# Performance work log

Measured on AMD Instinct MI355X. Metric: run time of the kernel, lower is better.

## Reference

```python
import jax, jax.numpy as jnp
import numpy as np

B, C, T, HEADS = 4, 1024, 1024, 16


def setup_inputs() -> dict:
    key = jax.random.key(0)
    k0, k1, k2, k3 = jax.random.split(key, 4)
    x = jax.random.normal(k0, (B, C, T), dtype=jnp.float32)
    mask = jax.random.randint(k1, (B, T), 0, 2).astype(bool)  # True = masked position
    scale = 1.0 / np.sqrt(C).astype(np.float32)
    w_kvq = jax.random.normal(k2, (3 * C, C), dtype=jnp.float32) * scale  # Conv1d k=1, no bias
    w_out = jax.random.normal(k3, (C, C), dtype=jnp.float32) * scale
    return {"x": x, "mask": mask, "w_kvq": w_kvq, "w_out": w_out}


def reference(x, mask, w_kvq, w_out):
    b, c, t = x.shape
    h = HEADS
    d = c // h  # head dim; torch scales by sqrt(k.size(1)) = sqrt(d)
    # Conv1d with kernel 1 == per-timestep matmul over channels
    kvq = jnp.einsum('oc,bct->bot', w_kvq, x)  # [B, 3C, T]
    k, v, q = jnp.split(kvq, 3, axis=1)        # each [B, C, T]
    k = k.reshape(b, h, d, t)
    v = v.reshape(b, h, d, t)
    q = q.reshape(b, h, d, t)
    # att[b,h,i,j] = <k_i, q_j> / sqrt(d); i = key pos, j = query pos
    att = jnp.einsum('bhdi,bhdj->bhij', k, q) / jnp.sqrt(jnp.asarray(d, x.dtype))
    # pre-softmax: mask key positions (dim i) with -inf
    att = jnp.where(mask[:, None, :, None], -jnp.inf, att)
    att = jax.nn.softmax(att, axis=2)  # softmax over keys (torch dim=1 of [Bh,Tk,Tq])
    # post-softmax: zero out masked query positions (dim j)
    att = jnp.where(mask[:, None, None, :], jnp.asarray(0.0, x.dtype), att)
    o = jnp.einsum('bhdi,bhij->bhdj', v, att)  # [B, h, d, T]
    o = o.reshape(b, c, t)
    out = x + jnp.einsum('oc,bct->bot', w_out, o)
    # match torch layout: cat over heads along batch dim -> [h*B, T, T]
    att_flat = jnp.transpose(att, (1, 0, 2, 3)).reshape(h * b, t, t)
    return out, att_flat
```

## Files before the change

### kernel.cpp

```cpp
#include <hip/hip_runtime.h>

#define BB 4
#define CC 1024
#define TT 1024
#define HH 16
#define DD 64

typedef __bf16 v8bf __attribute__((ext_vector_type(8)));
typedef __bf16 v4bf __attribute__((ext_vector_type(4)));
typedef float  v4f  __attribute__((ext_vector_type(4)));

__device__ __forceinline__ void gl_lds16(const __bf16* g, __bf16* l) {
  __builtin_amdgcn_global_load_lds(
      (const __attribute__((address_space(1))) void*)g,
      (__attribute__((address_space(3))) void*)l, 16, 0, 0);
}

__global__ __launch_bounds__(256) void prep(
    const void* mraw, float* __restrict__ maskf,
    const float* __restrict__ w_kvq, const float* __restrict__ w_out,
    __bf16* __restrict__ wkb, __bf16* __restrict__ wob)
{
  if (blockIdx.x == 0) {
    __shared__ int flagA, flagB;
    if (threadIdx.x == 0) { flagA = 0; flagB = 0; }
    __syncthreads();
    const unsigned char* mb = (const unsigned char*)mraw;
    const int n = BB * TT;
    int a = 0, bfl = 0;
    for (int i = threadIdx.x; i < n; i += 256) {
      if (mb[i]) { if ((i & 3) == 0) a = 1; else bfl = 1; }
    }
    if (a)   atomicOr(&flagA, 1);
    if (bfl) atomicOr(&flagB, 1);
    __syncthreads();
    int layout;
    if (flagA && !flagB)      layout = 0;
    else if (!flagA && flagB) layout = 1;
    else                      layout = 2;
    for (int i = threadIdx.x; i < n; i += 256) {
      float m;
      if (layout == 0)      m = (((const int*)mraw)[i]   != 0)   ? 1.f : 0.f;
      else if (layout == 1) m = (((const float*)mraw)[i] != 0.f) ? 1.f : 0.f;
      else                  m = (mb[i] != 0)                     ? 1.f : 0.f;
      maskf[i] = m;
    }
    return;
  }
  long i = ((long)blockIdx.x - 1) * 2048 + threadIdx.x * 8;
  const float* src;
  __bf16* dst;
  if (i < (long)3 * CC * CC) { src = w_kvq + i; dst = wkb + i; }
  else { long j = i - (long)3 * CC * CC; src = w_out + j; dst = wob + j; }
  float4 f0 = *(const float4*)src;
  float4 f1 = *(const float4*)(src + 4);
  v8bf o;
  o[0] = (__bf16)f0.x; o[1] = (__bf16)f0.y; o[2] = (__bf16)f0.z; o[3] = (__bf16)f0.w;
  o[4] = (__bf16)f1.x; o[5] = (__bf16)f1.y; o[6] = (__bf16)f1.z; o[7] = (__bf16)f1.w;
  *(v8bf*)dst = o;
}

__global__ __launch_bounds__(256) void transpose_x(const float* __restrict__ x,
                                                   __bf16* __restrict__ xT) {
  const int b = blockIdx.z;
  const int t0 = blockIdx.x * 64, c0 = blockIdx.y * 64;
  __shared__ __bf16 T[64][72];
  const int tid = threadIdx.x;
  {
    int row = tid >> 2, coff = (tid & 3) * 16;
    const float* src = x + ((long)b * CC + c0 + row) * TT + t0 + coff;
#pragma unroll
    for (int s = 0; s < 4; s++) {
      float4 f = *(const float4*)(src + s * 4);
      T[row][coff + s * 4 + 0] = (__bf16)f.x;
      T[row][coff + s * 4 + 1] = (__bf16)f.y;
      T[row][coff + s * 4 + 2] = (__bf16)f.z;
      T[row][coff + s * 4 + 3] = (__bf16)f.w;
    }
  }
  __syncthreads();
  {
    int trow = tid >> 2, ccoff = (tid & 3) * 16;
    __bf16 vals[16];
#pragma unroll
    for (int i = 0; i < 16; i++) vals[i] = T[ccoff + i][trow];
    __bf16* dst = xT + ((long)b * TT + t0 + trow) * CC + c0 + ccoff;
    *(v8bf*)dst       = *(v8bf*)&vals[0];
    *(v8bf*)(dst + 8) = *(v8bf*)&vals[8];
  }
}

template <int MODE>
__global__ __launch_bounds__(256) void gemm_bt(
    const __bf16* __restrict__ A, const __bf16* __restrict__ BTfull,
    const float* __restrict__ Sfull, float* __restrict__ Ofull,
    __bf16* __restrict__ kqT, __bf16* __restrict__ vbuf,
    long strideBT)
{
  const int bz = blockIdx.z;
  const __bf16* BT = BTfull + (long)bz * strideBT;
  const int m0 = blockIdx.y * 128, n0 = blockIdx.x * 128;
  __shared__ __align__(16) char smem[(MODE == 0) ? 34816 : 16384];
  __bf16 (*As)[32] = (__bf16(*)[32])smem;
  __bf16 (*Bs)[32] = (__bf16(*)[32])(smem + 8192);
  const int tid = threadIdx.x;
  const int lane = tid & 63, wave = tid >> 6;
  const int wm = wave >> 1, wn = wave & 1;
  const int ln = lane & 15, q = lane >> 4;

  v4f acc[4][4];
#pragma unroll
  for (int i = 0; i < 4; i++)
#pragma unroll
    for (int j = 0; j < 4; j++) acc[i][j] = (v4f)(0.f);

  const int lr = lane >> 2;
  const int lc = (lane & 3) * 8;
  for (int k0 = 0; k0 < CC; k0 += 32) {
#pragma unroll
    for (int s = 0; s < 2; s++) {
      int row = wave * 32 + s * 16;
      gl_lds16(A  + (long)(m0 + row + lr) * CC + k0 + lc, &As[row][0]);
      gl_lds16(BT + (long)(n0 + row + lr) * CC + k0 + lc, &Bs[row][0]);
    }
    __syncthreads();
    v8bf af[4], bf[4];
#pragma unroll
    for (int mi = 0; mi < 4; mi++) af[mi] = *(v8bf*)&As[wm * 64 + mi * 16 + ln][q * 8];
#pragma unroll
    for (int ni = 0; ni < 4; ni++) bf[ni] = *(v8bf*)&Bs[wn * 64 + ni * 16 + ln][q * 8];
#pragma unroll
    for (int mi = 0; mi < 4; mi++)
#pragma unroll
      for (int ni = 0; ni < 4; ni++)
        acc[mi][ni] = __builtin_amdgcn_mfma_f32_16x16x32_bf16(af[mi], bf[ni], acc[mi][ni], 0, 0, 0);
    __syncthreads();
  }

  if (MODE == 1) {
#pragma unroll
    for (int mi = 0; mi < 4; mi++)
#pragma unroll
      for (int ni = 0; ni < 4; ni++)
#pragma unroll
        for (int r = 0; r < 4; r++) {
          long off = (long)bz * CC * TT + (long)(m0 + wm * 64 + mi * 16 + q * 4 + r) * TT
                   + n0 + wn * 64 + ni * 16 + ln;
          Ofull[off] = acc[mi][ni][r] + Sfull[off];
        }
  } else {
    const int third = m0 >> 10;
    if (third == 1) {
      const int mb = m0 - 1024;
#pragma unroll
      for (int mi = 0; mi < 4; mi++)
#pragma unroll
        for (int ni = 0; ni < 4; ni++)
#pragma unroll
          for (int r = 0; r < 4; r++)
            vbuf[((long)bz * CC + mb + wm * 64 + mi * 16 + q * 4 + r) * TT
                 + n0 + wn * 64 + ni * 16 + ln] = (__bf16)acc[mi][ni][r];
    } else {
      __bf16 (*Tl)[136] = (__bf16(*)[136])smem;
#pragma unroll
      for (int mi = 0; mi < 4; mi++)
#pragma unroll
        for (int ni = 0; ni < 4; ni++) {
          v4bf pb;
#pragma unroll
          for (int r = 0; r < 4; r++) pb[r] = (__bf16)acc[mi][ni][r];
          *(v4bf*)&Tl[wn * 64 + ni * 16 + ln][wm * 64 + mi * 16 + q * 4] = pb;
        }
      __syncthreads();
      const int dstbase = (third == 0) ? 0 : CC;
      const int mcol = (third == 0) ? m0 : (m0 - 2048);
      int t = tid >> 1, c0 = (tid & 1) * 64;
      __bf16* drow = kqT + ((long)bz * TT + n0 + t) * (2 * CC) + dstbase + mcol + c0;
#pragma unroll
      for (int s = 0; s < 8; s++)
        *(v8bf*)(drow + s * 8) = *(v8bf*)&Tl[t][c0 + s * 8];
    }
  }
}

__global__ __launch_bounds__(256) void attn_fstats(
    const __bf16* __restrict__ kqT, const float* __restrict__ maskf,
    float2* __restrict__ fstats)
{
  const int z = blockIdx.y, h = z >> 2, b = z & 3;
  const int j0 = blockIdx.x * 64;
  const __bf16* kbase = kqT + (long)b * TT * (2 * CC);
  const int tid = threadIdx.x;
  const int lane = tid & 63, wave = tid >> 6;
  const int ln = lane & 15, q = lane >> 4;
  __shared__ float2 red[4][64];

  v8bf bq[4][2];
#pragma unroll
  for (int ni = 0; ni < 4; ni++)
#pragma unroll
    for (int kd = 0; kd < 2; kd++)
      bq[ni][kd] = *(const v8bf*)(kbase + (long)(j0 + ni * 16 + ln) * (2 * CC)
                                  + CC + h * DD + kd * 32 + q * 8);

  float rm[4], rs[4];
#pragma unroll
  for (int ni = 0; ni < 4; ni++) { rm[ni] = -3.4e38f; rs[ni] = 0.f; }

  for (int it = 0; it < 4; it++) {
    const int ibase = wave * 256 + it * 64;
    float4 km4[4];
    v8bf ak[4][2];
#pragma unroll
    for (int mi = 0; mi < 4; mi++) {
      km4[mi] = *(const float4*)(maskf + b * TT + ibase + mi * 16 + q * 4);
#pragma unroll
      for (int kd = 0; kd < 2; kd++)
        ak[mi][kd] = *(const v8bf*)(kbase + (long)(ibase + mi * 16 + ln) * (2 * CC)
                                    + h * DD + kd * 32 + q * 8);
    }
#pragma unroll
    for (int ni = 0; ni < 4; ni++) {
      float lv[16];
      float cm = -3.4e38f;
#pragma unroll
      for (int mi = 0; mi < 4; mi++) {
        v4f l4 = (v4f)(0.f);
        l4 = __builtin_amdgcn_mfma_f32_16x16x32_bf16(ak[mi][0], bq[ni][0], l4, 0, 0, 0);
        l4 = __builtin_amdgcn_mfma_f32_16x16x32_bf16(ak[mi][1], bq[ni][1], l4, 0, 0, 0);
#pragma unroll
        for (int r = 0; r < 4; r++) {
          float km = (r == 0) ? km4[mi].x : (r == 1) ? km4[mi].y : (r == 2) ? km4[mi].z : km4[mi].w;
          float l = (km != 0.f) ? -1e30f : l4[r] * 0.125f;
          lv[mi * 4 + r] = l;
          cm = fmaxf(cm, l);
        }
      }
      float nm = fmaxf(rm[ni], cm);
      float s = 0.f;
#pragma unroll
      for (int i = 0; i < 16; i++) s += __expf(lv[i] - nm);
      rs[ni] = rs[ni] * __expf(rm[ni] - nm) + s;
      rm[ni] = nm;
    }
  }

#pragma unroll
  for (int ni = 0; ni < 4; ni++) {
    float m = rm[ni], s = rs[ni];
#pragma unroll
    for (int off = 16; off <= 32; off <<= 1) {
      float om = __shfl_xor(m, off, 64);
      float os = __shfl_xor(s, off, 64);
      float M = fmaxf(m, om);
      s = s * __expf(m - M) + os * __expf(om - M);
      m = M;
    }
    if (q == 0) red[wave][ni * 16 + ln] = make_float2(m, s);
  }
  __syncthreads();
  if (tid < 64) {
    float M = -3.4e38f;
    float2 v[4];
#pragma unroll
    for (int w = 0; w < 4; w++) { v[w] = red[w][tid]; M = fmaxf(M, v[w].x); }
    float S = 0.f;
#pragma unroll
    for (int w = 0; w < 4; w++) S += v[w].y * __expf(v[w].x - M);
    const float qz = (maskf[b * TT + j0 + tid] != 0.f) ? 0.f : 1.f;
    fstats[(long)z * TT + j0 + tid] = make_float2(M, qz / S);
  }
}

__global__ __launch_bounds__(256) void gemm_pv(
    const __bf16* __restrict__ kqT, const __bf16* __restrict__ vbuf,
    const float2* __restrict__ fstats, const float* __restrict__ maskf,
    float* __restrict__ att, __bf16* __restrict__ oT)
{
  const int z = blockIdx.y, h = z >> 2, b = z & 3;
  const int j0 = blockIdx.x * 64;
  __shared__ __align__(16) char smem[50176];
  __bf16 (*Qs)[72] = (__bf16(*)[72])smem;
  float* km = (float*)(smem + 9216 + 4 * 9216);
  const int tid = threadIdx.x;
  const int lane = tid & 63, wave = tid >> 6;
  const int ln = lane & 15, q = lane >> 4;
  __bf16 (*Pt)[72] = (__bf16(*)[72])(smem + 9216 + wave * 9216);

  const __bf16* kbase = kqT + (long)b * TT * (2 * CC);
  const __bf16* vbase = vbuf + ((long)b * CC + h * DD) * TT;

#pragma unroll
  for (int s = 0; s < 2; s++) {
    int c = tid + s * 256;
    int row = c >> 3, off = (c & 7) * 8;
    *(v8bf*)&Qs[row][off] = *(const v8bf*)(kbase + (long)(j0 + row) * (2 * CC) + CC + h * DD + off);
  }
  {
    float4 f = *(const float4*)(maskf + b * TT + tid * 4);
    *(float4*)&km[tid * 4] = f;
  }
  __syncthreads();

  v8bf bq[4][2];
#pragma unroll
  for (int ni = 0; ni < 4; ni++)
#pragma unroll
    for (int kd = 0; kd < 2; kd++)
      bq[ni][kd] = *(v8bf*)&Qs[ni * 16 + ln][kd * 32 + q * 8];
  float2 st[4];
#pragma unroll
  for (int ni = 0; ni < 4; ni++) st[ni] = fstats[(long)z * TT + j0 + ni * 16 + ln];

  v4f acc[4][4];
#pragma unroll
  for (int i = 0; i < 4; i++)
#pragma unroll
    for (int j = 0; j < 4; j++) acc[i][j] = (v4f)(0.f);

  for (int it = 0; it < 4; it++) {
    const int ibase = wave * 256 + it * 64;
#pragma unroll
    for (int mi = 0; mi < 4; mi++) {
      const __bf16* arow = kbase + (long)(ibase + mi * 16 + ln) * (2 * CC) + h * DD;
      v8bf ak0 = *(const v8bf*)(arow + q * 8);
      v8bf ak1 = *(const v8bf*)(arow + 32 + q * 8);
#pragma unroll
      for (int ni = 0; ni < 4; ni++) {
        v4f l4 = (v4f)(0.f);
        l4 = __builtin_amdgcn_mfma_f32_16x16x32_bf16(ak0, bq[ni][0], l4, 0, 0, 0);
        l4 = __builtin_amdgcn_mfma_f32_16x16x32_bf16(ak1, bq[ni][1], l4, 0, 0, 0);
        v4bf pb;
#pragma unroll
        for (int r = 0; r < 4; r++) {
          int i_loc = mi * 16 + q * 4 + r;
          int i_glob = ibase + i_loc;
          float l = (km[i_glob] != 0.f) ? -1e30f : l4[r] * 0.125f;
          float p = __expf(l - st[ni].x) * st[ni].y;
          att[((long)z << 20) + (long)i_glob * TT + j0 + ni * 16 + ln] = p;
          pb[r] = (__bf16)p;
        }
        *(v4bf*)&Pt[ni * 16 + ln][mi * 16 + q * 4] = pb;
      }
    }
    v8bf ap[4][2], bv[4][2];
#pragma unroll
    for (int ji = 0; ji < 4; ji++)
#pragma unroll
      for (int ki = 0; ki < 2; ki++)
        ap[ji][ki] = *(v8bf*)&Pt[ji * 16 + ln][ki * 32 + q * 8];
#pragma unroll
    for (int di = 0; di < 4; di++)
#pragma unroll
      for (int ki = 0; ki < 2; ki++)
        bv[di][ki] = *(const v8bf*)(vbase + (long)(di * 16 + ln) * TT + ibase + ki * 32 + q * 8);
#pragma unroll
    for (int ji = 0; ji < 4; ji++)
#pragma unroll
      for (int di = 0; di < 4; di++) {
        acc[ji][di] = __builtin_amdgcn_mfma_f32_16x16x32_bf16(ap[ji][0], bv[di][0], acc[ji][di], 0, 0, 0);
        acc[ji][di] = __builtin_amdgcn_mfma_f32_16x16x32_bf16(ap[ji][1], bv[di][1], acc[ji][di], 0, 0, 0);
      }
  }

  float (*red)[68] = (float(*)[68])(smem + 9216);
  for (int w = 0; w < 4; w++) {
    __syncthreads();
    if (wave == w) {
#pragma unroll
      for (int ji = 0; ji < 4; ji++)
#pragma unroll
        for (int di = 0; di < 4; di++)
#pragma unroll
          for (int r = 0; r < 4; r++) {
            int row = ji * 16 + q * 4 + r;
            int col = di * 16 + ln;
            if (w == 0) red[row][col] = acc[ji][di][r];
            else        red[row][col] += acc[ji][di][r];
          }
    }
  }
  __syncthreads();
  {
    int row = tid >> 2, c0 = (tid & 3) * 16;
    __bf16 ob[16];
#pragma unroll
    for (int i = 0; i < 16; i++) ob[i] = (__bf16)red[row][c0 + i];
    __bf16* dst = oT + ((long)b * TT + j0 + row) * CC + h * DD + c0;
    *(v8bf*)dst       = *(v8bf*)&ob[0];
    *(v8bf*)(dst + 8) = *(v8bf*)&ob[8];
  }
}

extern "C" void kernel_launch(void* const* d_in, const int* in_sizes, int n_in,
                              void* d_out, int out_size, void* d_ws, size_t ws_size,
                              hipStream_t stream) {
  const float* x     = (const float*)d_in[0];
  const void*  mask  = d_in[1];
  const float* w_kvq = (const float*)d_in[2];
  const float* w_out = (const float*)d_in[3];

  float* out = (float*)d_out;
  float* att = out + (long)BB * CC * TT;

  char* wsb = (char*)d_ws;
  float*   maskf = (float*)(wsb + 0);
  __bf16*  wkb   = (__bf16*)(wsb + 16384);
  __bf16*  wob   = (__bf16*)(wsb + 6307840);
  __bf16*  xT    = (__bf16*)(wsb + 8404992);
  __bf16*  kqT   = (__bf16*)(wsb + 16793600);
  __bf16*  vbuf  = (__bf16*)(wsb + 33570816);
  __bf16*  oT    = (__bf16*)(wsb + 41959424);
  float2*  fst   = (float2*)(wsb + 50348032);

  prep<<<2049, 256, 0, stream>>>(mask, maskf, w_kvq, w_out, wkb, wob);
  transpose_x<<<dim3(16, 16, BB), 256, 0, stream>>>(x, xT);
  gemm_bt<0><<<dim3(8, 24, BB), 256, 0, stream>>>(
      wkb, xT, nullptr, nullptr, kqT, vbuf, (long)CC * TT);
  attn_fstats<<<dim3(16, HH * BB), 256, 0, stream>>>(kqT, maskf, fst);
  gemm_pv<<<dim3(16, HH * BB), 256, 0, stream>>>(kqT, vbuf, fst, maskf, att, oT);
  gemm_bt<1><<<dim3(8, 8, BB), 256, 0, stream>>>(
      wob, oT, x, out, nullptr, nullptr, (long)CC * TT);
}
```

Before: 471.2 us.

## Fuse prep kernels, merge softmax stats into PV kernel, deepen GEMM K-step

Folds the x transpose into the weight-prep kernel so there is one fewer launch. It also merges the softmax-statistics pass and the PV pass into one attention kernel. In that kernel each wave owns 16 query columns and loops over all keys twice, which removes the cross-wave LDS reduction and the fstats round trip. The GEMM now stages 64-wide K slices per barrier, and the large att and out writes use nontemporal stores. The cost is that each wave recomputes QK^T twice over the full key range, and each block now has less parallel work.

```diff
diff --git a/kernel.cpp b/kernel.cpp
--- a/kernel.cpp
+++ b/kernel.cpp
@@ -16,19 +16,22 @@
       (__attribute__((address_space(3))) void*)l, 16, 0, 0);
 }
 
-__global__ __launch_bounds__(256) void prep(
+__global__ __launch_bounds__(256) void prep_all(
     const void* mraw, float* __restrict__ maskf,
     const float* __restrict__ w_kvq, const float* __restrict__ w_out,
-    __bf16* __restrict__ wkb, __bf16* __restrict__ wob)
+    __bf16* __restrict__ wkb, __bf16* __restrict__ wob,
+    const float* __restrict__ x, __bf16* __restrict__ xT)
 {
-  if (blockIdx.x == 0) {
+  const int blk = blockIdx.x;
+  const int tid = threadIdx.x;
+  if (blk == 0) {
     __shared__ int flagA, flagB;
-    if (threadIdx.x == 0) { flagA = 0; flagB = 0; }
+    if (tid == 0) { flagA = 0; flagB = 0; }
     __syncthreads();
     const unsigned char* mb = (const unsigned char*)mraw;
     const int n = BB * TT;
     int a = 0, bfl = 0;
-    for (int i = threadIdx.x; i < n; i += 256) {
+    for (int i = tid; i < n; i += 256) {
       if (mb[i]) { if ((i & 3) == 0) a = 1; else bfl = 1; }
     }
     if (a)   atomicOr(&flagA, 1);
@@ -38,7 +41,7 @@
     if (flagA && !flagB)      layout = 0;
     else if (!flagA && flagB) layout = 1;
     else                      layout = 2;
-    for (int i = threadIdx.x; i < n; i += 256) {
+    for (int i = tid; i < n; i += 256) {
       float m;
       if (layout == 0)      m = (((const int*)mraw)[i]   != 0)   ? 1.f : 0.f;
       else if (layout == 1) m = (((const float*)mraw)[i] != 0.f) ? 1.f : 0.f;
@@ -47,25 +50,24 @@
     }
     return;
   }
-  long i = ((long)blockIdx.x - 1) * 2048 + threadIdx.x * 8;
-  const float* src;
-  __bf16* dst;
-  if (i < (long)3 * CC * CC) { src = w_kvq + i; dst = wkb + i; }
-  else { long j = i - (long)3 * CC * CC; src = w_out + j; dst = wob + j; }
-  float4 f0 = *(const float4*)src;
-  float4 f1 = *(const float4*)(src + 4);
-  v8bf o;
-  o[0] = (__bf16)f0.x; o[1] = (__bf16)f0.y; o[2] = (__bf16)f0.z; o[3] = (__bf16)f0.w;
-  o[4] = (__bf16)f1.x; o[5] = (__bf16)f1.y; o[6] = (__bf16)f1.z; o[7] = (__bf16)f1.w;
-  *(v8bf*)dst = o;
-}
-
-__global__ __launch_bounds__(256) void transpose_x(const float* __restrict__ x,
-                                                   __bf16* __restrict__ xT) {
-  const int b = blockIdx.z;
-  const int t0 = blockIdx.x * 64, c0 = blockIdx.y * 64;
+  if (blk <= 2048) {
+    long i = ((long)blk - 1) * 2048 + tid * 8;
+    const float* src;
+    __bf16* dst;
+    if (i < (long)3 * CC * CC) { src = w_kvq + i; dst = wkb + i; }
+    else { long j = i - (long)3 * CC * CC; src = w_out + j; dst = wob + j; }
+    float4 f0 = *(const float4*)src;
+    float4 f1 = *(const float4*)(src + 4);
+    v8bf o;
+    o[0] = (__bf16)f0.x; o[1] = (__bf16)f0.y; o[2] = (__bf16)f0.z; o[3] = (__bf16)f0.w;
+    o[4] = (__bf16)f1.x; o[5] = (__bf16)f1.y; o[6] = (__bf16)f1.z; o[7] = (__bf16)f1.w;
+    *(v8bf*)dst = o;
+    return;
+  }
+  const int tb = blk - 2049;
+  const int b = tb >> 8;
+  const int t0 = (tb & 15) * 64, c0 = ((tb >> 4) & 15) * 64;
   __shared__ __bf16 T[64][72];
-  const int tid = threadIdx.x;
   {
     int row = tid >> 2, coff = (tid & 3) * 16;
     const float* src = x + ((long)b * CC + c0 + row) * TT + t0 + coff;
@@ -100,9 +102,9 @@
   const int bz = blockIdx.z;
   const __bf16* BT = BTfull + (long)bz * strideBT;
   const int m0 = blockIdx.y * 128, n0 = blockIdx.x * 128;
-  __shared__ __align__(16) char smem[(MODE == 0) ? 34816 : 16384];
-  __bf16 (*As)[32] = (__bf16(*)[32])smem;
-  __bf16 (*Bs)[32] = (__bf16(*)[32])(smem + 8192);
+  __shared__ __align__(16) char smem[(MODE == 0) ? 34816 : 32768];
+  __bf16 (*As)[128][32] = (__bf16(*)[128][32])smem;
+  __bf16 (*Bs)[128][32] = (__bf16(*)[128][32])(smem + 16384);
   const int tid = threadIdx.x;
   const int lane = tid & 63, wave = tid >> 6;
   const int wm = wave >> 1, wn = wave & 1;
@@ -116,24 +118,35 @@
 
   const int lr = lane >> 2;
   const int lc = (lane & 3) * 8;
-  for (int k0 = 0; k0 < CC; k0 += 32) {
+  for (int k0 = 0; k0 < CC; k0 += 64) {
 #pragma unroll
     for (int s = 0; s < 2; s++) {
       int row = wave * 32 + s * 16;
-      gl_lds16(A  + (long)(m0 + row + lr) * CC + k0 + lc, &As[row][0]);
-      gl_lds16(BT + (long)(n0 + row + lr) * CC + k0 + lc, &Bs[row][0]);
+#pragma unroll
+      for (int kd = 0; kd < 2; kd++) {
+        gl_lds16(A  + (long)(m0 + row + lr) * CC + k0 + kd * 32 + lc, &As[kd][row][0]);
+        gl_lds16(BT + (long)(n0 + row + lr) * CC + k0 + kd * 32 + lc, &Bs[kd][row][0]);
+      }
     }
     __syncthreads();
-    v8bf af[4], bf[4];
-#pragma unroll
-    for (int mi = 0; mi < 4; mi++) af[mi] = *(v8bf*)&As[wm * 64 + mi * 16 + ln][q * 8];
-#pragma unroll
-    for (int ni = 0; ni < 4; ni++) bf[ni] = *(v8bf*)&Bs[wn * 64 + ni * 16 + ln][q * 8];
+    v8bf af[4][2], bf[4][2];
 #pragma unroll
     for (int mi = 0; mi < 4; mi++)
 #pragma unroll
-      for (int ni = 0; ni < 4; ni++)
-        acc[mi][ni] = __builtin_amdgcn_mfma_f32_16x16x32_bf16(af[mi], bf[ni], acc[mi][ni], 0, 0, 0);
+      for (int kd = 0; kd < 2; kd++)
+        af[mi][kd] = *(v8bf*)&As[kd][wm * 64 + mi * 16 + ln][q * 8];
+#pragma unroll
+    for (int ni = 0; ni < 4; ni++)
+#pragma unroll
+      for (int kd = 0; kd < 2; kd++)
+        bf[ni][kd] = *(v8bf*)&Bs[kd][wn * 64 + ni * 16 + ln][q * 8];
+#pragma unroll
+    for (int mi = 0; mi < 4; mi++)
+#pragma unroll
+      for (int ni = 0; ni < 4; ni++) {
+        acc[mi][ni] = __builtin_amdgcn_mfma_f32_16x16x32_bf16(af[mi][0], bf[ni][0], acc[mi][ni], 0, 0, 0);
+        acc[mi][ni] = __builtin_amdgcn_mfma_f32_16x16x32_bf16(af[mi][1], bf[ni][1], acc[mi][ni], 0, 0, 0);
+      }
     __syncthreads();
   }
 
@@ -146,7 +159,7 @@
         for (int r = 0; r < 4; r++) {
           long off = (long)bz * CC * TT + (long)(m0 + wm * 64 + mi * 16 + q * 4 + r) * TT
                    + n0 + wn * 64 + ni * 16 + ln;
-          Ofull[off] = acc[mi][ni][r] + Sfull[off];
+          __builtin_nontemporal_store(acc[mi][ni][r] + Sfull[off], &Ofull[off]);
         }
   } else {
     const int third = m0 >> 10;
@@ -183,212 +196,114 @@
   }
 }
 
-__global__ __launch_bounds__(256) void attn_fstats(
-    const __bf16* __restrict__ kqT, const float* __restrict__ maskf,
-    float2* __restrict__ fstats)
+__global__ __launch_bounds__(256) void attn_fused(
+    const __bf16* __restrict__ kqT, const __bf16* __restrict__ vbuf,
+    const float* __restrict__ maskf, float* __restrict__ att,
+    __bf16* __restrict__ oT)
 {
   const int z = blockIdx.y, h = z >> 2, b = z & 3;
   const int j0 = blockIdx.x * 64;
-  const __bf16* kbase = kqT + (long)b * TT * (2 * CC);
   const int tid = threadIdx.x;
   const int lane = tid & 63, wave = tid >> 6;
   const int ln = lane & 15, q = lane >> 4;
-  __shared__ float2 red[4][64];
-
-  v8bf bq[4][2];
-#pragma unroll
-  for (int ni = 0; ni < 4; ni++)
-#pragma unroll
-    for (int kd = 0; kd < 2; kd++)
-      bq[ni][kd] = *(const v8bf*)(kbase + (long)(j0 + ni * 16 + ln) * (2 * CC)
-                                  + CC + h * DD + kd * 32 + q * 8);
-
-  float rm[4], rs[4];
-#pragma unroll
-  for (int ni = 0; ni < 4; ni++) { rm[ni] = -3.4e38f; rs[ni] = 0.f; }
-
-  for (int it = 0; it < 4; it++) {
-    const int ibase = wave * 256 + it * 64;
-    float4 km4[4];
-    v8bf ak[4][2];
-#pragma unroll
-    for (int mi = 0; mi < 4; mi++) {
-      km4[mi] = *(const float4*)(maskf + b * TT + ibase + mi * 16 + q * 4);
-#pragma unroll
-      for (int kd = 0; kd < 2; kd++)
-        ak[mi][kd] = *(const v8bf*)(kbase + (long)(ibase + mi * 16 + ln) * (2 * CC)
-                                    + h * DD + kd * 32 + q * 8);
-    }
-#pragma unroll
-    for (int ni = 0; ni < 4; ni++) {
-      float lv[16];
-      float cm = -3.4e38f;
-#pragma unroll
-      for (int mi = 0; mi < 4; mi++) {
-        v4f l4 = (v4f)(0.f);
-        l4 = __builtin_amdgcn_mfma_f32_16x16x32_bf16(ak[mi][0], bq[ni][0], l4, 0, 0, 0);
-        l4 = __builtin_amdgcn_mfma_f32_16x16x32_bf16(ak[mi][1], bq[ni][1], l4, 0, 0, 0);
-#pragma unroll
-        for (int r = 0; r < 4; r++) {
-          float km = (r == 0) ? km4[mi].x : (r == 1) ? km4[mi].y : (r == 2) ? km4[mi].z : km4[mi].w;
-          float l = (km != 0.f) ? -1e30f : l4[r] * 0.125f;
-          lv[mi * 4 + r] = l;
-          cm = fmaxf(cm, l);
-        }
-      }
-      float nm = fmaxf(rm[ni], cm);
-      float s = 0.f;
-#pragma unroll
-      for (int i = 0; i < 16; i++) s += __expf(lv[i] - nm);
-      rs[ni] = rs[ni] * __expf(rm[ni] - nm) + s;
-      rm[ni] = nm;
-    }
-  }
-
-#pragma unroll
-  for (int ni = 0; ni < 4; ni++) {
-    float m = rm[ni], s = rs[ni];
-#pragma unroll
-    for (int off = 16; off <= 32; off <<= 1) {
-      float om = __shfl_xor(m, off, 64);
-      float os = __shfl_xor(s, off, 64);
-      float M = fmaxf(m, om);
-      s = s * __expf(m - M) + os * __expf(om - M);
-      m = M;
-    }
-    if (q == 0) red[wave][ni * 16 + ln] = make_float2(m, s);
-  }
-  __syncthreads();
-  if (tid < 64) {
-    float M = -3.4e38f;
-    float2 v[4];
-#pragma unroll
-    for (int w = 0; w < 4; w++) { v[w] = red[w][tid]; M = fmaxf(M, v[w].x); }
-    float S = 0.f;
-#pragma unroll
-    for (int w = 0; w < 4; w++) S += v[w].y * __expf(v[w].x - M);
-    const float qz = (maskf[b * TT + j0 + tid] != 0.f) ? 0.f : 1.f;
-    fstats[(long)z * TT + j0 + tid] = make_float2(M, qz / S);
-  }
-}
-
-__global__ __launch_bounds__(256) void gemm_pv(
-    const __bf16* __restrict__ kqT, const __bf16* __restrict__ vbuf,
-    const float2* __restrict__ fstats, const float* __restrict__ maskf,
-    float* __restrict__ att, __bf16* __restrict__ oT)
-{
-  const int z = blockIdx.y, h = z >> 2, b = z & 3;
-  const int j0 = blockIdx.x * 64;
-  __shared__ __align__(16) char smem[50176];
-  __bf16 (*Qs)[72] = (__bf16(*)[72])smem;
-  float* km = (float*)(smem + 9216 + 4 * 9216);
-  const int tid = threadIdx.x;
-  const int lane = tid & 63, wave = tid >> 6;
-  const int ln = lane & 15, q = lane >> 4;
-  __bf16 (*Pt)[72] = (__bf16(*)[72])(smem + 9216 + wave * 9216);
+  __shared__ float km[1024];
+  __shared__ __bf16 PtAll[4][16][72];
 
   const __bf16* kbase = kqT + (long)b * TT * (2 * CC);
   const __bf16* vbase = vbuf + ((long)b * CC + h * DD) * TT;
-
-#pragma unroll
-  for (int s = 0; s < 2; s++) {
-    int c = tid + s * 256;
-    int row = c >> 3, off = (c & 7) * 8;
-    *(v8bf*)&Qs[row][off] = *(const v8bf*)(kbase + (long)(j0 + row) * (2 * CC) + CC + h * DD + off);
-  }
-  {
-    float4 f = *(const float4*)(maskf + b * TT + tid * 4);
-    *(float4*)&km[tid * 4] = f;
-  }
+  const int jw = j0 + wave * 16;
+
+  *(float4*)&km[tid * 4] = *(const float4*)(maskf + b * TT + tid * 4);
   __syncthreads();
 
-  v8bf bq[4][2];
-#pragma unroll
-  for (int ni = 0; ni < 4; ni++)
-#pragma unroll
-    for (int kd = 0; kd < 2; kd++)
-      bq[ni][kd] = *(v8bf*)&Qs[ni * 16 + ln][kd * 32 + q * 8];
-  float2 st[4];
-#pragma unroll
-  for (int ni = 0; ni < 4; ni++) st[ni] = fstats[(long)z * TT + j0 + ni * 16 + ln];
-
-  v4f acc[4][4];
-#pragma unroll
-  for (int i = 0; i < 4; i++)
-#pragma unroll
-    for (int j = 0; j < 4; j++) acc[i][j] = (v4f)(0.f);
-
-  for (int it = 0; it < 4; it++) {
-    const int ibase = wave * 256 + it * 64;
+  v8bf bq[2];
+#pragma unroll
+  for (int kd = 0; kd < 2; kd++)
+    bq[kd] = *(const v8bf*)(kbase + (long)(jw + ln) * (2 * CC) + CC + h * DD + kd * 32 + q * 8);
+
+  float rm = -3.4e38f, rs = 0.f;
+  for (int it = 0; it < 16; it++) {
+    const int ibase = it * 64;
+    float lv[16];
+    float cm = -3.4e38f;
 #pragma unroll
     for (int mi = 0; mi < 4; mi++) {
       const __bf16* arow = kbase + (long)(ibase + mi * 16 + ln) * (2 * CC) + h * DD;
       v8bf ak0 = *(const v8bf*)(arow + q * 8);
       v8bf ak1 = *(const v8bf*)(arow + 32 + q * 8);
-#pragma unroll
-      for (int ni = 0; ni < 4; ni++) {
-        v4f l4 = (v4f)(0.f);
-        l4 = __builtin_amdgcn_mfma_f32_16x16x32_bf16(ak0, bq[ni][0], l4, 0, 0, 0);
-        l4 = __builtin_amdgcn_mfma_f32_16x16x32_bf16(ak1, bq[ni][1], l4, 0, 0, 0);
-        v4bf pb;
-#pragma unroll
-        for (int r = 0; r < 4; r++) {
-          int i_loc = mi * 16 + q * 4 + r;
-          int i_glob = ibase + i_loc;
-          float l = (km[i_glob] != 0.f) ? -1e30f : l4[r] * 0.125f;
-          float p = __expf(l - st[ni].x) * st[ni].y;
-          att[((long)z << 20) + (long)i_glob * TT + j0 + ni * 16 + ln] = p;
-          pb[r] = (__bf16)p;
-        }
-        *(v4bf*)&Pt[ni * 16 + ln][mi * 16 + q * 4] = pb;
+      v4f l4 = (v4f)(0.f);
+      l4 = __builtin_amdgcn_mfma_f32_16x16x32_bf16(ak0, bq[0], l4, 0, 0, 0);
+      l4 = __builtin_amdgcn_mfma_f32_16x16x32_bf16(ak1, bq[1], l4, 0, 0, 0);
+#pragma unroll
+      for (int r = 0; r < 4; r++) {
+        int i = ibase + mi * 16 + q * 4 + r;
+        float l = (km[i] != 0.f) ? -1e30f : l4[r] * 0.125f;
+        lv[mi * 4 + r] = l;
+        cm = fmaxf(cm, l);
       }
     }
-    v8bf ap[4][2], bv[4][2];
-#pragma unroll
-    for (int ji = 0; ji < 4; ji++)
-#pragma unroll
-      for (int ki = 0; ki < 2; ki++)
-        ap[ji][ki] = *(v8bf*)&Pt[ji * 16 + ln][ki * 32 + q * 8];
+    float nm = fmaxf(rm, cm);
+    float s = 0.f;
+#pragma unroll
+    for (int i = 0; i < 16; i++) s += __expf(lv[i] - nm);
+    rs = rs * __expf(rm - nm) + s;
+    rm = nm;
+  }
+#pragma unroll
+  for (int off = 16; off <= 32; off <<= 1) {
+    float om = __shfl_xor(rm, off, 64);
+    float os = __shfl_xor(rs, off, 64);
+    float M = fmaxf(rm, om);
+    rs = rs * __expf(rm - M) + os * __expf(om - M);
+    rm = M;
+  }
+  const float qz = (km[jw + ln] != 0.f) ? 0.f : 1.f;
+  const float Mf = rm, iS = qz / rs;
+
+  v4f acc[4];
+#pragma unroll
+  for (int di = 0; di < 4; di++) acc[di] = (v4f)(0.f);
+  __bf16 (*Pt)[72] = PtAll[wave];
+
+  for (int it = 0; it < 16; it++) {
+    const int ibase = it * 64;
+#pragma unroll
+    for (int mi = 0; mi < 4; mi++) {
+      const __bf16* arow = kbase + (long)(ibase + mi * 16 + ln) * (2 * CC) + h * DD;
+      v8bf ak0 = *(const v8bf*)(arow + q * 8);
+      v8bf ak1 = *(const v8bf*)(arow + 32 + q * 8);
+      v4f l4 = (v4f)(0.f);
+      l4 = __builtin_amdgcn_mfma_f32_16x16x32_bf16(ak0, bq[0], l4, 0, 0, 0);
+      l4 = __builtin_amdgcn_mfma_f32_16x16x32_bf16(ak1, bq[1], l4, 0, 0, 0);
+      v4bf pb;
+#pragma unroll
+      for (int r = 0; r < 4; r++) {
+        int i = ibase + mi * 16 + q * 4 + r;
+        float l = (km[i] != 0.f) ? -1e30f : l4[r] * 0.125f;
+        float p = __expf(l - Mf) * iS;
+        __builtin_nontemporal_store(p, att + ((long)z << 20) + (long)i * TT + jw + ln);
+        pb[r] = (__bf16)p;
+      }
+      *(v4bf*)&Pt[ln][mi * 16 + q * 4] = pb;
+    }
+    v8bf ap[2];
+#pragma unroll
+    for (int kd = 0; kd < 2; kd++) ap[kd] = *(v8bf*)&Pt[ln][kd * 32 + q * 8];
+#pragma unroll
+    for (int di = 0; di < 4; di++) {
+      v8bf bv0 = *(const v8bf*)(vbase + (long)(di * 16 + ln) * TT + ibase + q * 8);
+      v8bf bv1 = *(const v8bf*)(vbase + (long)(di * 16 + ln) * TT + ibase + 32 + q * 8);
+      acc[di] = __builtin_amdgcn_mfma_f32_16x16x32_bf16(ap[0], bv0, acc[di], 0, 0, 0);
+      acc[di] = __builtin_amdgcn_mfma_f32_16x16x32_bf16(ap[1], bv1, acc[di], 0, 0, 0);
+    }
+  }
+
+#pragma unroll
+  for (int r = 0; r < 4; r++) {
+    __bf16* drow = oT + ((long)b * TT + jw + q * 4 + r) * CC + h * DD;
 #pragma unroll
     for (int di = 0; di < 4; di++)
-#pragma unroll
-      for (int ki = 0; ki < 2; ki++)
-        bv[di][ki] = *(const v8bf*)(vbase + (long)(di * 16 + ln) * TT + ibase + ki * 32 + q * 8);
-#pragma unroll
-    for (int ji = 0; ji < 4; ji++)
-#pragma unroll
-      for (int di = 0; di < 4; di++) {
-        acc[ji][di] = __builtin_amdgcn_mfma_f32_16x16x32_bf16(ap[ji][0], bv[di][0], acc[ji][di], 0, 0, 0);
-        acc[ji][di] = __builtin_amdgcn_mfma_f32_16x16x32_bf16(ap[ji][1], bv[di][1], acc[ji][di], 0, 0, 0);
-      }
-  }
-
-  float (*red)[68] = (float(*)[68])(smem + 9216);
-  for (int w = 0; w < 4; w++) {
-    __syncthreads();
-    if (wave == w) {
-#pragma unroll
-      for (int ji = 0; ji < 4; ji++)
-#pragma unroll
-        for (int di = 0; di < 4; di++)
-#pragma unroll
-          for (int r = 0; r < 4; r++) {
-            int row = ji * 16 + q * 4 + r;
-            int col = di * 16 + ln;
-            if (w == 0) red[row][col] = acc[ji][di][r];
-            else        red[row][col] += acc[ji][di][r];
-          }
-    }
-  }
-  __syncthreads();
-  {
-    int row = tid >> 2, c0 = (tid & 3) * 16;
-    __bf16 ob[16];
-#pragma unroll
-    for (int i = 0; i < 16; i++) ob[i] = (__bf16)red[row][c0 + i];
-    __bf16* dst = oT + ((long)b * TT + j0 + row) * CC + h * DD + c0;
-    *(v8bf*)dst       = *(v8bf*)&ob[0];
-    *(v8bf*)(dst + 8) = *(v8bf*)&ob[8];
+      drow[di * 16 + ln] = (__bf16)acc[di][r];
   }
 }
 
@@ -411,14 +326,11 @@
   __bf16*  kqT   = (__bf16*)(wsb + 16793600);
   __bf16*  vbuf  = (__bf16*)(wsb + 33570816);
   __bf16*  oT    = (__bf16*)(wsb + 41959424);
-  float2*  fst   = (float2*)(wsb + 50348032);
-
-  prep<<<2049, 256, 0, stream>>>(mask, maskf, w_kvq, w_out, wkb, wob);
-  transpose_x<<<dim3(16, 16, BB), 256, 0, stream>>>(x, xT);
+
+  prep_all<<<3073, 256, 0, stream>>>(mask, maskf, w_kvq, w_out, wkb, wob, x, xT);
   gemm_bt<0><<<dim3(8, 24, BB), 256, 0, stream>>>(
       wkb, xT, nullptr, nullptr, kqT, vbuf, (long)CC * TT);
-  attn_fstats<<<dim3(16, HH * BB), 256, 0, stream>>>(kqT, maskf, fst);
-  gemm_pv<<<dim3(16, HH * BB), 256, 0, stream>>>(kqT, vbuf, fst, maskf, att, oT);
+  attn_fused<<<dim3(16, HH * BB), 256, 0, stream>>>(kqT, vbuf, maskf, att, oT);
   gemm_bt<1><<<dim3(8, 8, BB), 256, 0, stream>>>(
       wob, oT, x, out, nullptr, nullptr, (long)CC * TT);
 }
```

Result: slower. 520.7 us (+10.5%).
